# Kernel optimization log

Measured on AMD Instinct MI355X. Metric: run time of the kernel, lower is better.

Reference implementation:

```python
import jax, jax.numpy as jnp
import numpy as np
from jax.ops import segment_sum, segment_max

N = 100000   # nodes
E = 1000000  # edges
G = 100      # graphs in batch
NF, EF = 9, 2
FT, FE = 3, 8
HID = 64
H, C = 4, 16          # heads, per-head channels (H*C == HID, concat=True)
LAT = 32
L = 3                 # num GAT layers
NEG_SLOPE = 0.2       # PyG GATConv LeakyReLU slope


def setup_inputs() -> dict:
    key = jax.random.key(0)
    ks = jax.random.split(key, 20)
    def nrm(k, shp, s=0.05):
        return jax.random.normal(k, shp, jnp.float32) * s
    return dict(
        x=jax.random.normal(ks[0], (N, NF), jnp.float32),
        face_types=jax.random.randint(ks[1], (N,), 0, FT),
        edge_index=jax.random.randint(ks[2], (2, E), 0, N),
        edge_attr=jax.random.normal(ks[3], (E, EF), jnp.float32),
        batch=jnp.sort(jax.random.randint(ks[4], (N,), 0, G)),
        node_mask=jnp.ones((N,), jnp.float32),
        num_graphs=G,
        face_emb=nrm(ks[5], (FT, FE)),
        node_W=nrm(ks[6], (NF + FE, HID)), node_b=jnp.zeros((HID,), jnp.float32),
        edge_W=nrm(ks[7], (EF, HID)), edge_b=jnp.zeros((HID,), jnp.float32),
        gat_lin=nrm(ks[8], (L, HID, HID)),
        gat_lin_edge=nrm(ks[9], (L, HID, HID)),
        gat_att_src=nrm(ks[10], (L, H, C)),
        gat_att_dst=nrm(ks[11], (L, H, C)),
        gat_att_edge=nrm(ks[12], (L, H, C)),
        gat_bias=jnp.zeros((L, HID), jnp.float32),
        mu_W=nrm(ks[13], (HID, LAT)), mu_b=jnp.zeros((LAT,), jnp.float32),
        lv_W=nrm(ks[14], (HID, LAT)), lv_b=jnp.zeros((LAT,), jnp.float32),
    )


def _gat(h, src, dst, edge_h, W, We, a_s, a_d, a_e, b):
    """PyG GATConv (eval): shared lin, self-loops with fill_value='mean', segment softmax over dst."""
    n = h.shape[0]
    xh = (h @ W).reshape(n, H, C)                       # (N,H,C)
    al_s = (xh * a_s).sum(-1)                           # (N,H)
    al_d = (xh * a_d).sum(-1)                           # (N,H)
    # self-loop edge_attr = mean of incoming encoded edge features (fill_value='mean')
    deg = segment_sum(jnp.ones((src.shape[0],), h.dtype), dst, num_segments=n)
    loop_attr = segment_sum(edge_h, dst, num_segments=n) / jnp.clip(deg, 1.0)[:, None]
    loops = jnp.arange(n)
    sa = jnp.concatenate([src, loops])                  # (E+N,)
    da = jnp.concatenate([dst, loops])
    ea = jnp.concatenate([edge_h, loop_attr], axis=0)   # (E+N,HID)
    eh = (ea @ We).reshape(-1, H, C)
    al_e = (eh * a_e).sum(-1)                           # (E+N,H)
    alpha = jax.nn.leaky_relu(al_s[sa] + al_d[da] + al_e, NEG_SLOPE)
    amax = segment_max(alpha, da, num_segments=n)       # every node has a self-loop -> no empty segment
    ex = jnp.exp(alpha - amax[da])
    denom = segment_sum(ex, da, num_segments=n)
    w = ex / denom[da]                                  # (E+N,H)
    out = segment_sum(xh[sa] * w[:, :, None], da, num_segments=n)  # (N,H,C)
    return out.reshape(n, H * C) + b


def reference(x, face_types, edge_index, edge_attr, batch, node_mask, num_graphs,
              face_emb, node_W, node_b, edge_W, edge_b,
              gat_lin, gat_lin_edge, gat_att_src, gat_att_dst, gat_att_edge, gat_bias,
              mu_W, mu_b, lv_W, lv_b):
    h = jax.nn.relu(jnp.concatenate([x, face_emb[face_types]], axis=-1) @ node_W + node_b)
    edge_h = jax.nn.relu(edge_attr @ edge_W + edge_b)
    src, dst = edge_index[0], edge_index[1]
    for l in range(gat_lin.shape[0]):
        h = jax.nn.relu(_gat(h, src, dst, edge_h, gat_lin[l], gat_lin_edge[l],
                             gat_att_src[l], gat_att_dst[l], gat_att_edge[l], gat_bias[l]))
    # masked scatter-mean pooling per graph
    hm = h * node_mask[:, None]
    h_sum = segment_sum(hm, batch, num_segments=num_graphs)
    counts = segment_sum(node_mask, batch, num_segments=num_graphs)
    hp = h_sum / jnp.clip(counts, 1.0)[:, None]
    mu = hp @ mu_W + mu_b
    logvar = hp @ lv_W + lv_b
    return mu, logvar
```

## Files before the change

### kernel.cpp

```cpp
#include <hip/hip_runtime.h>
#include <math.h>

#define NN 100000
#define NE 1000000
#define NG 100
#define NL 3
#define NEG 0.2f

__device__ __forceinline__ float lrelu(float x){ return fmaxf(x, NEG*x); }

__global__ void k_ve(const float* __restrict__ We, const float* __restrict__ ae,
                     float* __restrict__ Ve2){
  int i = blockIdx.x*blockDim.x + threadIdx.x;
  if(i >= NL*4*64) return;
  int d = i & 63, h = (i>>6)&3, l = i>>8;
  const float* w = We + l*4096 + d*64 + h*16;
  const float* a = ae + l*64 + h*16;
  float s = 0.f;
  #pragma unroll
  for(int c=0;c<16;c++) s = fmaf(w[c], a[c], s);
  Ve2[(l*4+h)*64 + d] = s;
}

__global__ void k_h0(const float* __restrict__ x, const int* __restrict__ ft,
                     const float* __restrict__ femb, const float* __restrict__ W,
                     const float* __restrict__ b, float* __restrict__ h){
  int i = blockIdx.x*blockDim.x + threadIdx.x;
  if(i >= NN*64) return;
  int n = i>>6, d = i&63;
  const float* xr = x + (size_t)n*9;
  const float* fe = femb + ft[n]*8;
  float s = b[d];
  #pragma unroll
  for(int k=0;k<9;k++) s = fmaf(xr[k], W[k*64+d], s);
  #pragma unroll
  for(int j=0;j<8;j++) s = fmaf(fe[j], W[(9+j)*64+d], s);
  h[i] = fmaxf(s, 0.f);
}

__global__ void k_deg(const int* __restrict__ dst, int* __restrict__ deg){
  int e = blockIdx.x*blockDim.x + threadIdx.x;
  if(e < NE) atomicAdd(&deg[dst[e]], 1);
}

__global__ void k_scan1(const int* __restrict__ deg, int* __restrict__ rp,
                        int* __restrict__ bsum){
  __shared__ int sd[256];
  int t = threadIdx.x;
  int base = blockIdx.x*1024 + t*4;
  int v0 = (base+0<NN)?deg[base+0]:0;
  int v1 = (base+1<NN)?deg[base+1]:0;
  int v2 = (base+2<NN)?deg[base+2]:0;
  int v3 = (base+3<NN)?deg[base+3]:0;
  int ts = v0+v1+v2+v3;
  sd[t] = ts; __syncthreads();
  for(int off=1; off<256; off<<=1){
    int add = (t>=off)? sd[t-off] : 0;
    __syncthreads();
    sd[t] += add;
    __syncthreads();
  }
  int excl = sd[t] - ts;
  if(t==255) bsum[blockIdx.x] = sd[t];
  if(base+0<NN) rp[base+0]=excl;
  if(base+1<NN) rp[base+1]=excl+v0;
  if(base+2<NN) rp[base+2]=excl+v0+v1;
  if(base+3<NN) rp[base+3]=excl+v0+v1+v2;
}
__global__ void k_scan2(int* __restrict__ bsum, int nb){
  if(threadIdx.x==0 && blockIdx.x==0){
    int acc=0;
    for(int i=0;i<nb;i++){ int v=bsum[i]; bsum[i]=acc; acc+=v; }
  }
}
__global__ void k_scan3(int* __restrict__ rp, const int* __restrict__ bsum){
  int i = blockIdx.x*blockDim.x + threadIdx.x;
  if(i < NN) rp[i] += bsum[i>>10];
  if(i == 0) rp[NN] = NE;
}

__global__ void k_edge(const float* __restrict__ eattr, const int* __restrict__ src,
                       const int* __restrict__ dst, const float* __restrict__ eW,
                       const float* __restrict__ eb, const float* __restrict__ Ve2,
                       const int* __restrict__ rp, int* __restrict__ fill,
                       int* __restrict__ csrc, float* __restrict__ cal){
  int e = blockIdx.x*blockDim.x + threadIdx.x;
  if(e >= NE) return;
  float a0 = eattr[(size_t)e*2], a1 = eattr[(size_t)e*2+1];
  float acc[12];
  #pragma unroll
  for(int t=0;t<12;t++) acc[t]=0.f;
  #pragma unroll 4
  for(int d=0; d<64; d+=4){
    float4 w0 = *(const float4*)&eW[d];
    float4 w1 = *(const float4*)&eW[64+d];
    float4 bb = *(const float4*)&eb[d];
    float4 eh;
    eh.x = fmaxf(fmaf(a0, w0.x, fmaf(a1, w1.x, bb.x)), 0.f);
    eh.y = fmaxf(fmaf(a0, w0.y, fmaf(a1, w1.y, bb.y)), 0.f);
    eh.z = fmaxf(fmaf(a0, w0.z, fmaf(a1, w1.z, bb.z)), 0.f);
    eh.w = fmaxf(fmaf(a0, w0.w, fmaf(a1, w1.w, bb.w)), 0.f);
    #pragma unroll
    for(int j=0;j<12;j++){
      float4 v = *(const float4*)&Ve2[j*64 + d];
      acc[j] = fmaf(eh.x, v.x, acc[j]);
      acc[j] = fmaf(eh.y, v.y, acc[j]);
      acc[j] = fmaf(eh.z, v.z, acc[j]);
      acc[j] = fmaf(eh.w, v.w, acc[j]);
    }
  }
  int dd = dst[e];
  int pos = rp[dd] + atomicAdd(&fill[dd], 1);
  csrc[pos] = src[e];
  *(float4*)&cal[(size_t)pos*4]              = make_float4(acc[0], acc[1], acc[2],  acc[3]);
  *(float4*)&cal[((size_t)NE   + pos)*4]     = make_float4(acc[4], acc[5], acc[6],  acc[7]);
  *(float4*)&cal[((size_t)NE*2 + pos)*4]     = make_float4(acc[8], acc[9], acc[10], acc[11]);
}

__global__ __launch_bounds__(256) void k_xh(
    const float* __restrict__ hin, const float* __restrict__ W,
    const float* __restrict__ aS, const float* __restrict__ aD,
    float* __restrict__ xh, float* __restrict__ alsd){
  __shared__ float hs[64][68];
  __shared__ float Ws[64][64];
  int t  = threadIdx.x;
  int td = t & 15;
  int tn = t >> 4;
  int n0 = blockIdx.x*64;
  size_t base = (size_t)n0*64;
  #pragma unroll
  for(int i=0;i<4;i++){
    int idx4 = t + i*256;
    int row  = idx4 >> 4;
    int c4   = (idx4 & 15)*4;
    float4 hv = make_float4(0.f,0.f,0.f,0.f);
    if(base + (size_t)idx4*4 < (size_t)NN*64)
      hv = *(const float4*)&hin[base + (size_t)idx4*4];
    *(float4*)&hs[row][c4] = hv;
    *(float4*)&Ws[row][c4] = *(const float4*)&W[(size_t)idx4*4];
  }
  __syncthreads();

  float acc[4][4];
  #pragma unroll
  for(int i=0;i<4;i++)
    #pragma unroll
    for(int j=0;j<4;j++) acc[i][j]=0.f;

  for(int k=0;k<64;k+=4){
    float4 w0 = *(float4*)&Ws[k+0][td*4];
    float4 w1 = *(float4*)&Ws[k+1][td*4];
    float4 w2 = *(float4*)&Ws[k+2][td*4];
    float4 w3 = *(float4*)&Ws[k+3][td*4];
    #pragma unroll
    for(int i=0;i<4;i++){
      float4 hv = *(float4*)&hs[tn*4+i][k];
      acc[i][0] = fmaf(hv.x, w0.x, acc[i][0]);
      acc[i][1] = fmaf(hv.x, w0.y, acc[i][1]);
      acc[i][2] = fmaf(hv.x, w0.z, acc[i][2]);
      acc[i][3] = fmaf(hv.x, w0.w, acc[i][3]);
      acc[i][0] = fmaf(hv.y, w1.x, acc[i][0]);
      acc[i][1] = fmaf(hv.y, w1.y, acc[i][1]);
      acc[i][2] = fmaf(hv.y, w1.z, acc[i][2]);
      acc[i][3] = fmaf(hv.y, w1.w, acc[i][3]);
      acc[i][0] = fmaf(hv.z, w2.x, acc[i][0]);
      acc[i][1] = fmaf(hv.z, w2.y, acc[i][1]);
      acc[i][2] = fmaf(hv.z, w2.z, acc[i][2]);
      acc[i][3] = fmaf(hv.z, w2.w, acc[i][3]);
      acc[i][0] = fmaf(hv.w, w3.x, acc[i][0]);
      acc[i][1] = fmaf(hv.w, w3.y, acc[i][1]);
      acc[i][2] = fmaf(hv.w, w3.z, acc[i][2]);
      acc[i][3] = fmaf(hv.w, w3.w, acc[i][3]);
    }
  }

  float as0 = aS[td*4+0], as1 = aS[td*4+1], as2 = aS[td*4+2], as3 = aS[td*4+3];
  float ad0 = aD[td*4+0], ad1 = aD[td*4+1], ad2 = aD[td*4+2], ad3 = aD[td*4+3];
  int head = td>>2;

  #pragma unroll
  for(int i=0;i<4;i++){
    int n = n0 + tn*4 + i;
    if(n >= NN) break;
    *(float4*)&xh[(size_t)n*64 + td*4] =
        make_float4(acc[i][0], acc[i][1], acc[i][2], acc[i][3]);
    float vs = acc[i][0]*as0 + acc[i][1]*as1 + acc[i][2]*as2 + acc[i][3]*as3;
    float vd = acc[i][0]*ad0 + acc[i][1]*ad1 + acc[i][2]*ad2 + acc[i][3]*ad3;
    vs += __shfl_xor(vs, 1); vs += __shfl_xor(vs, 2);
    vd += __shfl_xor(vd, 1); vd += __shfl_xor(vd, 2);
    if((td&3)==0){
      alsd[(size_t)n*8 + head]     = vs;
      alsd[(size_t)n*8 + 4 + head] = vd;
    }
  }
}

__global__ __launch_bounds__(256) void k_gat(
    const float* __restrict__ xh, const float* __restrict__ alsd,
    const int* __restrict__ rp, const int* __restrict__ csrc,
    const float* __restrict__ cal, const float* __restrict__ bias,
    float* __restrict__ hout){
  int d = threadIdx.x & 63, h = d>>4;
  int n = __builtin_amdgcn_readfirstlane(blockIdx.x*4 + (threadIdx.x>>6));
  if(n >= NN) return;
  int r0 = rp[n], r1 = rp[n+1];
  int dg = r1 - r0;
  float alD_n = alsd[(size_t)n*8 + 4 + h];
  float m = -1e30f, den = 0.f, acc = 0.f, sum_al = 0.f;
  int p = r0;
  for(; p+4 <= r1; p += 4){
    int s0 = csrc[p+0];
    int s1 = csrc[p+1];
    int s2 = csrc[p+2];
    int s3 = csrc[p+3];
    float e0 = cal[(size_t)(p+0)*4 + h];
    float e1 = cal[(size_t)(p+1)*4 + h];
    float e2 = cal[(size_t)(p+2)*4 + h];
    float e3 = cal[(size_t)(p+3)*4 + h];
    float a0 = alsd[(size_t)s0*8 + h];
    float a1 = alsd[(size_t)s1*8 + h];
    float a2 = alsd[(size_t)s2*8 + h];
    float a3 = alsd[(size_t)s3*8 + h];
    float x0 = xh[(size_t)s0*64 + d];
    float x1 = xh[(size_t)s1*64 + d];
    float x2 = xh[(size_t)s2*64 + d];
    float x3 = xh[(size_t)s3*64 + d];
    sum_al += e0 + e1 + e2 + e3;
    float l0 = lrelu(a0 + alD_n + e0);
    float l1 = lrelu(a1 + alD_n + e1);
    float l2 = lrelu(a2 + alD_n + e2);
    float l3 = lrelu(a3 + alD_n + e3);
    float pmax = fmaxf(fmaxf(l0, l1), fmaxf(l2, l3));
    if(pmax > m + 8.f){
      float sc = __expf(m - pmax);
      den *= sc; acc *= sc; m = pmax;
    }
    float w0 = __expf(l0 - m); den += w0; acc = fmaf(w0, x0, acc);
    float w1 = __expf(l1 - m); den += w1; acc = fmaf(w1, x1, acc);
    float w2 = __expf(l2 - m); den += w2; acc = fmaf(w2, x2, acc);
    float w3 = __expf(l3 - m); den += w3; acc = fmaf(w3, x3, acc);
  }
  for(; p < r1; p++){
    int s = csrc[p];
    float e = cal[(size_t)p*4 + h];
    float as = alsd[(size_t)s*8 + h];
    float xv = xh[(size_t)s*64 + d];
    sum_al += e;
    float lg = lrelu(as + alD_n + e);
    if(lg > m + 8.f){
      float sc = __expf(m - lg);
      den *= sc; acc *= sc; m = lg;
    }
    float w = __expf(lg - m); den += w; acc = fmaf(w, xv, acc);
  }
  float alS_n = alsd[(size_t)n*8 + h];
  float loop_al = dg>0 ? sum_al/(float)dg : 0.f;
  float la = lrelu(alS_n + alD_n + loop_al);
  float nm = fmaxf(m, la);
  float sc = __expf(m - nm);
  float wl = __expf(la - nm);
  den = den*sc + wl;
  acc = fmaf(wl, xh[(size_t)n*64+d], acc*sc);
  hout[(size_t)n*64+d] = fmaxf(acc/den + bias[d], 0.f);
}

__global__ void k_pool(const float* __restrict__ h, const int* __restrict__ batch,
                       const float* __restrict__ mask, float* __restrict__ hsum,
                       float* __restrict__ cnt){
  int d = threadIdx.x;
  int start = blockIdx.x*64;
  if(start >= NN) return;
  int end = min(start+64, NN);
  int curg = batch[start];
  float acc = 0.f, c = 0.f;
  for(int n=start; n<end; n++){
    int g = batch[n];
    if(g != curg){
      atomicAdd(&hsum[(size_t)curg*64+d], acc);
      if(d==0) atomicAdd(&cnt[curg], c);
      acc = 0.f; c = 0.f; curg = g;
    }
    float mk = mask[n];
    acc = fmaf(h[(size_t)n*64+d], mk, acc);
    if(d==0) c += mk;
  }
  atomicAdd(&hsum[(size_t)curg*64+d], acc);
  if(d==0) atomicAdd(&cnt[curg], c);
}

__global__ void k_final(const float* __restrict__ hsum, const float* __restrict__ cnt,
                        const float* __restrict__ muW, const float* __restrict__ mub,
                        const float* __restrict__ lvW, const float* __restrict__ lvb,
                        float* __restrict__ out){
  int i = blockIdx.x*blockDim.x + threadIdx.x;
  if(i >= NG*32*2) return;
  int which = i / (NG*32);
  int r = i % (NG*32);
  int g = r >> 5, j = r & 31;
  float rc = 1.f / fmaxf(cnt[g], 1.f);
  const float* W = which ? lvW : muW;
  float s = which ? lvb[j] : mub[j];
  const float* hr = hsum + (size_t)g*64;
  #pragma unroll 8
  for(int k=0;k<64;k++) s = fmaf(hr[k]*rc, W[k*32+j], s);
  out[i] = s;
}

extern "C" void kernel_launch(void* const* d_in, const int* in_sizes, int n_in,
                              void* d_out, int out_size, void* d_ws, size_t ws_size,
                              hipStream_t stream){
  const float* x      = (const float*)d_in[0];
  const int*   ft     = (const int*)d_in[1];
  const int*   ei     = (const int*)d_in[2];
  const float* eattr  = (const float*)d_in[3];
  const int*   batch  = (const int*)d_in[4];
  const float* mask   = (const float*)d_in[5];
  const float* femb   = (const float*)d_in[7];
  const float* nW     = (const float*)d_in[8];
  const float* nb     = (const float*)d_in[9];
  const float* eW     = (const float*)d_in[10];
  const float* ebias  = (const float*)d_in[11];
  const float* glin   = (const float*)d_in[12];
  const float* gline  = (const float*)d_in[13];
  const float* aS     = (const float*)d_in[14];
  const float* aD     = (const float*)d_in[15];
  const float* aE     = (const float*)d_in[16];
  const float* gbias  = (const float*)d_in[17];
  const float* muW    = (const float*)d_in[18];
  const float* mub    = (const float*)d_in[19];
  const float* lvW    = (const float*)d_in[20];
  const float* lvb    = (const float*)d_in[21];
  const int* src = ei;
  const int* dstp = ei + NE;

  char* ws = (char*)d_ws;
  size_t off = 0;
  auto alloc = [&](size_t bytes)->void*{
    void* p = ws + off; off += (bytes + 255) & ~(size_t)255; return p;
  };
  int*   deg  = (int*)  alloc((size_t)NN*4);
  int*   fill = (int*)  alloc((size_t)NN*4);
  int*   rp   = (int*)  alloc((size_t)(NN+1)*4);
  int*   bsum = (int*)  alloc(128*4);
  int*   csrc = (int*)  alloc((size_t)NE*4);
  float* cal  = (float*)alloc((size_t)NL*NE*4*4);
  float* alsd = (float*)alloc((size_t)NN*8*4);
  float* Ve2  = (float*)alloc((size_t)NL*4*64*4);
  float* hbuf = (float*)alloc((size_t)NN*64*4);
  float* xb   = (float*)alloc((size_t)NN*64*4);
  float* hsum = (float*)alloc((size_t)NG*64*4);
  float* cnt  = (float*)alloc((size_t)NG*4);

  hipMemsetAsync(deg,  0, (size_t)NN*4, stream);
  hipMemsetAsync(fill, 0, (size_t)NN*4, stream);
  hipMemsetAsync(hsum, 0, (size_t)NG*64*4, stream);
  hipMemsetAsync(cnt,  0, (size_t)NG*4, stream);

  k_ve  <<<3, 256, 0, stream>>>(gline, aE, Ve2);
  k_h0  <<<(NN*64+255)/256, 256, 0, stream>>>(x, ft, femb, nW, nb, hbuf);
  k_deg <<<(NE+255)/256, 256, 0, stream>>>(dstp, deg);
  k_scan1<<<(NN+1023)/1024, 256, 0, stream>>>(deg, rp, bsum);
  k_scan2<<<1, 64, 0, stream>>>(bsum, (NN+1023)/1024);
  k_scan3<<<(NN+255)/256, 256, 0, stream>>>(rp, bsum);
  k_edge<<<(NE+255)/256, 256, 0, stream>>>(eattr, src, dstp, eW, ebias, Ve2,
                                           rp, fill, csrc, cal);

  for(int l=0;l<NL;l++){
    k_xh <<<(NN+63)/64, 256, 0, stream>>>(hbuf, glin + (size_t)l*4096,
                                          aS + l*64, aD + l*64, xb, alsd);
    k_gat<<<(NN+3)/4, 256, 0, stream>>>(xb, alsd, rp, csrc,
                                        cal + (size_t)l*NE*4, gbias + l*64, hbuf);
  }
  k_pool <<<(NN+63)/64, 64, 0, stream>>>(hbuf, batch, mask, hsum, cnt);
  k_final<<<(NG*32*2+255)/256, 256, 0, stream>>>(hsum, cnt, muW, mub, lvW, lvb,
                                                 (float*)d_out);
}
```

Baseline: 436.1 us.

## Pre-bucket edges by destination block before computing edge attention scatter

Result: slower. 768.7 us (+76.3%).

```diff
diff --git a/kernel.cpp b/kernel.cpp
--- a/kernel.cpp
+++ b/kernel.cpp
@@ -6,6 +6,7 @@
 #define NG 100
 #define NL 3
 #define NEG 0.2f
+#define NB ((NN + 255) / 256)
 
 __device__ __forceinline__ float lrelu(float x){ return fmaxf(x, NEG*x); }
 
@@ -79,14 +80,33 @@
   if(i == 0) rp[NN] = NE;
 }
 
-__global__ void k_edge(const float* __restrict__ eattr, const int* __restrict__ src,
-                       const int* __restrict__ dst, const float* __restrict__ eW,
+__global__ void k_bucket(const int* __restrict__ src, const int* __restrict__ dst,
+                         const float* __restrict__ eattr, const int* __restrict__ rp,
+                         int* __restrict__ bfill, float4* __restrict__ bucket){
+  int e = blockIdx.x*blockDim.x + threadIdx.x;
+  if(e >= NE) return;
+  int dd = dst[e];
+  int b = dd >> 8;
+  int w = atomicAdd(&bfill[b], 1);
+  int base = rp[b << 8];
+  float4 r;
+  r.x = __int_as_float(src[e]);
+  r.y = __int_as_float(dd);
+  r.z = eattr[(size_t)e*2];
+  r.w = eattr[(size_t)e*2+1];
+  bucket[(size_t)base + w] = r;
+}
+
+__global__ void k_edge(const float4* __restrict__ bucket, const float* __restrict__ eW,
                        const float* __restrict__ eb, const float* __restrict__ Ve2,
                        const int* __restrict__ rp, int* __restrict__ fill,
                        int* __restrict__ csrc, float* __restrict__ cal){
   int e = blockIdx.x*blockDim.x + threadIdx.x;
   if(e >= NE) return;
-  float a0 = eattr[(size_t)e*2], a1 = eattr[(size_t)e*2+1];
+  float4 r = bucket[e];
+  int ss = __float_as_int(r.x);
+  int dd = __float_as_int(r.y);
+  float a0 = r.z, a1 = r.w;
   float acc[12];
   #pragma unroll
   for(int t=0;t<12;t++) acc[t]=0.f;
@@ -109,12 +129,11 @@
       acc[j] = fmaf(eh.w, v.w, acc[j]);
     }
   }
-  int dd = dst[e];
   int pos = rp[dd] + atomicAdd(&fill[dd], 1);
-  csrc[pos] = src[e];
-  *(float4*)&cal[(size_t)pos*4]              = make_float4(acc[0], acc[1], acc[2],  acc[3]);
-  *(float4*)&cal[((size_t)NE   + pos)*4]     = make_float4(acc[4], acc[5], acc[6],  acc[7]);
-  *(float4*)&cal[((size_t)NE*2 + pos)*4]     = make_float4(acc[8], acc[9], acc[10], acc[11]);
+  csrc[pos] = ss;
+  *(float4*)&cal[(size_t)pos*4]          = make_float4(acc[0], acc[1], acc[2],  acc[3]);
+  *(float4*)&cal[((size_t)NE   + pos)*4] = make_float4(acc[4], acc[5], acc[6],  acc[7]);
+  *(float4*)&cal[((size_t)NE*2 + pos)*4] = make_float4(acc[8], acc[9], acc[10], acc[11]);
 }
 
 __global__ __launch_bounds__(256) void k_xh(
@@ -338,23 +357,26 @@
   auto alloc = [&](size_t bytes)->void*{
     void* p = ws + off; off += (bytes + 255) & ~(size_t)255; return p;
   };
-  int*   deg  = (int*)  alloc((size_t)NN*4);
-  int*   fill = (int*)  alloc((size_t)NN*4);
-  int*   rp   = (int*)  alloc((size_t)(NN+1)*4);
-  int*   bsum = (int*)  alloc(128*4);
-  int*   csrc = (int*)  alloc((size_t)NE*4);
-  float* cal  = (float*)alloc((size_t)NL*NE*4*4);
-  float* alsd = (float*)alloc((size_t)NN*8*4);
-  float* Ve2  = (float*)alloc((size_t)NL*4*64*4);
-  float* hbuf = (float*)alloc((size_t)NN*64*4);
-  float* xb   = (float*)alloc((size_t)NN*64*4);
-  float* hsum = (float*)alloc((size_t)NG*64*4);
-  float* cnt  = (float*)alloc((size_t)NG*4);
-
-  hipMemsetAsync(deg,  0, (size_t)NN*4, stream);
-  hipMemsetAsync(fill, 0, (size_t)NN*4, stream);
-  hipMemsetAsync(hsum, 0, (size_t)NG*64*4, stream);
-  hipMemsetAsync(cnt,  0, (size_t)NG*4, stream);
+  int*    deg    = (int*)   alloc((size_t)NN*4);
+  int*    fill   = (int*)   alloc((size_t)NN*4);
+  int*    bfill  = (int*)   alloc((size_t)NB*4);
+  int*    rp     = (int*)   alloc((size_t)(NN+1)*4);
+  int*    bsum   = (int*)   alloc(128*4);
+  float4* bucket = (float4*)alloc((size_t)NE*16);
+  int*    csrc   = (int*)   alloc((size_t)NE*4);
+  float*  cal    = (float*) alloc((size_t)NL*NE*4*4);
+  float*  alsd   = (float*) alloc((size_t)NN*8*4);
+  float*  Ve2    = (float*) alloc((size_t)NL*4*64*4);
+  float*  hbuf   = (float*) alloc((size_t)NN*64*4);
+  float*  xb     = (float*) alloc((size_t)NN*64*4);
+  float*  hsum   = (float*) alloc((size_t)NG*64*4);
+  float*  cnt    = (float*) alloc((size_t)NG*4);
+
+  hipMemsetAsync(deg,   0, (size_t)NN*4, stream);
+  hipMemsetAsync(fill,  0, (size_t)NN*4, stream);
+  hipMemsetAsync(bfill, 0, (size_t)NB*4, stream);
+  hipMemsetAsync(hsum,  0, (size_t)NG*64*4, stream);
+  hipMemsetAsync(cnt,   0, (size_t)NG*4, stream);
 
   k_ve  <<<3, 256, 0, stream>>>(gline, aE, Ve2);
   k_h0  <<<(NN*64+255)/256, 256, 0, stream>>>(x, ft, femb, nW, nb, hbuf);
@@ -362,7 +384,8 @@
   k_scan1<<<(NN+1023)/1024, 256, 0, stream>>>(deg, rp, bsum);
   k_scan2<<<1, 64, 0, stream>>>(bsum, (NN+1023)/1024);
   k_scan3<<<(NN+255)/256, 256, 0, stream>>>(rp, bsum);
-  k_edge<<<(NE+255)/256, 256, 0, stream>>>(eattr, src, dstp, eW, ebias, Ve2,
+  k_bucket<<<(NE+255)/256, 256, 0, stream>>>(src, dstp, eattr, rp, bfill, bucket);
+  k_edge<<<(NE+255)/256, 256, 0, stream>>>(bucket, eW, ebias, Ve2,
                                            rp, fill, csrc, cal);
 
   for(int l=0;l<NL;l++){
```

## Split each node's GAT edge list across two waves and merge softmax state

Applied to the files above, without the earlier changes.

Result: slower. 520.8 us (+19.4%).

```diff
diff --git a/kernel.cpp b/kernel.cpp
--- a/kernel.cpp
+++ b/kernel.cpp
@@ -39,8 +39,13 @@
 }
 
 __global__ void k_deg(const int* __restrict__ dst, int* __restrict__ deg){
-  int e = blockIdx.x*blockDim.x + threadIdx.x;
-  if(e < NE) atomicAdd(&deg[dst[e]], 1);
+  int i = blockIdx.x*blockDim.x + threadIdx.x;
+  if(i >= NE/4) return;
+  #pragma unroll
+  for(int k=0;k<4;k++){
+    int e = i + k*(NE/4);
+    atomicAdd(&deg[dst[e]], 1);
+  }
 }
 
 __global__ void k_scan1(const int* __restrict__ deg, int* __restrict__ rp,
@@ -112,9 +117,9 @@
   int dd = dst[e];
   int pos = rp[dd] + atomicAdd(&fill[dd], 1);
   csrc[pos] = src[e];
-  *(float4*)&cal[(size_t)pos*4]              = make_float4(acc[0], acc[1], acc[2],  acc[3]);
-  *(float4*)&cal[((size_t)NE   + pos)*4]     = make_float4(acc[4], acc[5], acc[6],  acc[7]);
-  *(float4*)&cal[((size_t)NE*2 + pos)*4]     = make_float4(acc[8], acc[9], acc[10], acc[11]);
+  *(float4*)&cal[(size_t)pos*4]          = make_float4(acc[0], acc[1], acc[2],  acc[3]);
+  *(float4*)&cal[((size_t)NE   + pos)*4] = make_float4(acc[4], acc[5], acc[6],  acc[7]);
+  *(float4*)&cal[((size_t)NE*2 + pos)*4] = make_float4(acc[8], acc[9], acc[10], acc[11]);
 }
 
 __global__ __launch_bounds__(256) void k_xh(
@@ -200,15 +205,23 @@
     const int* __restrict__ rp, const int* __restrict__ csrc,
     const float* __restrict__ cal, const float* __restrict__ bias,
     float* __restrict__ hout){
-  int d = threadIdx.x & 63, h = d>>4;
-  int n = __builtin_amdgcn_readfirstlane(blockIdx.x*4 + (threadIdx.x>>6));
-  if(n >= NN) return;
+  __shared__ float sm[2][64][4];
+  int t = threadIdx.x;
+  int wid  = t >> 6;
+  int lane = t & 63;
+  int d = lane, h = d >> 4;
+  int half = wid & 1;
+  int slot = wid >> 1;
+  int n = __builtin_amdgcn_readfirstlane(blockIdx.x*2 + slot);
   int r0 = rp[n], r1 = rp[n+1];
   int dg = r1 - r0;
+  int mid = r0 + ((dg + 1) >> 1);
+  int pa = half ? mid : r0;
+  int pb = half ? r1  : mid;
   float alD_n = alsd[(size_t)n*8 + 4 + h];
   float m = -1e30f, den = 0.f, acc = 0.f, sum_al = 0.f;
-  int p = r0;
-  for(; p+4 <= r1; p += 4){
+  int p = pa;
+  for(; p+4 <= pb; p += 4){
     int s0 = csrc[p+0];
     int s1 = csrc[p+1];
     int s2 = csrc[p+2];
@@ -240,7 +253,7 @@
     float w2 = __expf(l2 - m); den += w2; acc = fmaf(w2, x2, acc);
     float w3 = __expf(l3 - m); den += w3; acc = fmaf(w3, x3, acc);
   }
-  for(; p < r1; p++){
+  for(; p < pb; p++){
     int s = csrc[p];
     float e = cal[(size_t)p*4 + h];
     float as = alsd[(size_t)s*8 + h];
@@ -253,6 +266,24 @@
     }
     float w = __expf(lg - m); den += w; acc = fmaf(w, xv, acc);
   }
+  if(half == 1){
+    sm[slot][lane][0] = m;
+    sm[slot][lane][1] = den;
+    sm[slot][lane][2] = acc;
+    sm[slot][lane][3] = sum_al;
+  }
+  __syncthreads();
+  if(half == 1) return;
+  float m2   = sm[slot][lane][0];
+  float den2 = sm[slot][lane][1];
+  float acc2 = sm[slot][lane][2];
+  sum_al    += sm[slot][lane][3];
+  float M  = fmaxf(m, m2);
+  float f1 = __expf(m - M);
+  float f2 = __expf(m2 - M);
+  den = den*f1 + den2*f2;
+  acc = acc*f1 + acc2*f2;
+  m = M;
   float alS_n = alsd[(size_t)n*8 + h];
   float loop_al = dg>0 ? sum_al/(float)dg : 0.f;
   float la = lrelu(alS_n + alD_n + loop_al);
@@ -338,18 +369,18 @@
   auto alloc = [&](size_t bytes)->void*{
     void* p = ws + off; off += (bytes + 255) & ~(size_t)255; return p;
   };
-  int*   deg  = (int*)  alloc((size_t)NN*4);
-  int*   fill = (int*)  alloc((size_t)NN*4);
-  int*   rp   = (int*)  alloc((size_t)(NN+1)*4);
-  int*   bsum = (int*)  alloc(128*4);
-  int*   csrc = (int*)  alloc((size_t)NE*4);
-  float* cal  = (float*)alloc((size_t)NL*NE*4*4);
-  float* alsd = (float*)alloc((size_t)NN*8*4);
-  float* Ve2  = (float*)alloc((size_t)NL*4*64*4);
-  float* hbuf = (float*)alloc((size_t)NN*64*4);
-  float* xb   = (float*)alloc((size_t)NN*64*4);
-  float* hsum = (float*)alloc((size_t)NG*64*4);
-  float* cnt  = (float*)alloc((size_t)NG*4);
+  int*    deg   = (int*)   alloc((size_t)NN*4);
+  int*    fill  = (int*)   alloc((size_t)NN*4);
+  int*    rp    = (int*)   alloc((size_t)(NN+1)*4);
+  int*    bsum  = (int*)   alloc(128*4);
+  int*    csrc  = (int*)   alloc((size_t)NE*4);
+  float*  cal   = (float*) alloc((size_t)NL*NE*4*4);
+  float*  alsd  = (float*) alloc((size_t)NN*8*4);
+  float*  Ve2   = (float*) alloc((size_t)NL*4*64*4);
+  float*  hbuf  = (float*) alloc((size_t)NN*64*4);
+  float*  xb    = (float*) alloc((size_t)NN*64*4);
+  float*  hsum  = (float*) alloc((size_t)NG*64*4);
+  float*  cnt   = (float*) alloc((size_t)NG*4);
 
   hipMemsetAsync(deg,  0, (size_t)NN*4, stream);
   hipMemsetAsync(fill, 0, (size_t)NN*4, stream);
@@ -358,7 +389,7 @@
 
   k_ve  <<<3, 256, 0, stream>>>(gline, aE, Ve2);
   k_h0  <<<(NN*64+255)/256, 256, 0, stream>>>(x, ft, femb, nW, nb, hbuf);
-  k_deg <<<(NE+255)/256, 256, 0, stream>>>(dstp, deg);
+  k_deg <<<(NE/4+255)/256, 256, 0, stream>>>(dstp, deg);
   k_scan1<<<(NN+1023)/1024, 256, 0, stream>>>(deg, rp, bsum);
   k_scan2<<<1, 64, 0, stream>>>(bsum, (NN+1023)/1024);
   k_scan3<<<(NN+255)/256, 256, 0, stream>>>(rp, bsum);
@@ -368,8 +399,8 @@
   for(int l=0;l<NL;l++){
     k_xh <<<(NN+63)/64, 256, 0, stream>>>(hbuf, glin + (size_t)l*4096,
                                           aS + l*64, aD + l*64, xb, alsd);
-    k_gat<<<(NN+3)/4, 256, 0, stream>>>(xb, alsd, rp, csrc,
-                                        cal + (size_t)l*NE*4, gbias + l*64, hbuf);
+    k_gat<<<NN/2, 256, 0, stream>>>(xb, alsd, rp, csrc,
+                                    cal + (size_t)l*NE*4, gbias + l*64, hbuf);
   }
   k_pool <<<(NN+63)/64, 64, 0, stream>>>(hbuf, batch, mask, hsum, cnt);
   k_final<<<(NG*32*2+255)/256, 256, 0, stream>>>(hsum, cnt, muW, mub, lvW, lvb,
```
